# Optimization experiments

Hardware: AMD Instinct MI355X
Metric: run time of the kernel (lower is better)

## Reference

```python
import jax, jax.numpy as jnp
import numpy as np

EPS = 1e-4


def _linear_scan(a, b):
    # y_t = a_t * y_{t-1} + b_t ; a: [L], b: [L, d]
    def combine(c1, c2):
        a1, b1 = c1
        a2, b2 = c2
        return a1 * a2, a2[..., None] * b1 + b2
    _, y = jax.lax.associative_scan(combine, (a, b))
    return y


def setup_inputs() -> dict:
    key = jax.random.key(0)
    k1, k2, k3 = jax.random.split(key, 3)
    L_inner, d, n_seqs = 131072, 512, 8
    h_flat = jax.random.normal(k1, (L_inner, d), dtype=jnp.float32)
    p_selected_flat = jax.random.uniform(k2, (L_inner,), dtype=jnp.float32)
    # outer stream: alternating boundary mask -> cumsum-1 indexes stay in [0, L_inner-1]
    b_flat = jnp.tile(jnp.array([1, 0], dtype=jnp.int32), L_inner)  # [2*L_inner]
    h_seq_idx = jnp.sort(jax.random.randint(k3, (1, L_inner), 0, n_seqs)).astype(jnp.int32)
    return {"h_flat": h_flat, "b_flat": b_flat,
            "p_selected_flat": p_selected_flat, "h_seq_idx": h_seq_idx}


def reference(h_flat, b_flat, p_selected_flat, h_seq_idx):
    # dt derivation: p clamped, dt = -log(1-p); x = h / dt (cast round-trip as in torch)
    p = jnp.clip(p_selected_flat.astype(jnp.float32), EPS, 1.0 - EPS)
    dt = -jnp.log1p(-p)                                   # [L]
    x = (h_flat.astype(jnp.float32) / dt[:, None]).astype(h_flat.dtype).astype(jnp.float32)
    # mamba_chunk_scan_combined with A=-1, B=p, C=1, dstate=1 reduces to:
    #   state_t = exp(-dt_t) * state_{t-1} + dt_t * p_t * x_t ; y_t = state_t
    # with state reset at seq_idx segment boundaries.
    seq = h_seq_idx[0]
    start = jnp.concatenate([jnp.array([True]), seq[1:] != seq[:-1]])
    a = jnp.where(start, 0.0, jnp.exp(-dt))               # decay (== 1-p), reset at starts
    b = (dt * p)[:, None] * x                             # [L, d] input term (== p*h)
    z_bar = _linear_scan(a, b).astype(h_flat.dtype)       # [L_inner, d]
    # dechunk expand: each outer token reads the state of its latest chunk
    idx = jnp.cumsum(b_flat) - 1                          # [L_outer]
    return z_bar[idx]
```

## Files before the change

kernel.cpp:

```cpp
#include <hip/hip_runtime.h>
#include <math.h>

#define EPSV 1e-4f
#define SCHUNK 64

__device__ __forceinline__ float agent_load_f(const float* p) {
    return __hip_atomic_load(p, __ATOMIC_RELAXED, __HIP_MEMORY_SCOPE_AGENT);
}
__device__ __forceinline__ void agent_store_f(float* p, float v) {
    __hip_atomic_store(p, v, __ATOMIC_RELAXED, __HIP_MEMORY_SCOPE_AGENT);
}
__device__ __forceinline__ int agent_load_i(const int* p) {
    return __hip_atomic_load(p, __ATOMIC_RELAXED, __HIP_MEMORY_SCOPE_AGENT);
}
__device__ __forceinline__ void agent_store_i(int* p, int v) {
    __hip_atomic_store(p, v, __ATOMIC_RELAXED, __HIP_MEMORY_SCOPE_AGENT);
}

__global__ void clear_kernel(int* __restrict__ flags, int n) {
    int i = blockIdx.x * blockDim.x + threadIdx.x;
    if (i < n) flags[i] = 0;
}

__global__ void scan_sum_kernel(const int* __restrict__ b, int n,
                                int* __restrict__ bsum) {
    __shared__ int red[256];
    int tid = threadIdx.x;
    int base = blockIdx.x * 1024 + tid * 4;
    int s = 0;
#pragma unroll
    for (int k = 0; k < 4; ++k) {
        int j = base + k;
        if (j < n) s += b[j];
    }
    red[tid] = s;
    __syncthreads();
    for (int off = 128; off > 0; off >>= 1) {
        if (tid < off) red[tid] += red[tid + off];
        __syncthreads();
    }
    if (tid == 0) bsum[blockIdx.x] = red[0];
}

__global__ void scan_offsets_kernel(const int* __restrict__ bsum,
                                    int* __restrict__ boff, int nb) {
    __shared__ int sh[1024];
    int i = threadIdx.x;
    int v = (i < nb) ? bsum[i] : 0;
    sh[i] = v;
    __syncthreads();
    for (int off = 1; off < 1024; off <<= 1) {
        int t = sh[i];
        if (i >= off) t += sh[i - off];
        __syncthreads();
        sh[i] = t;
        __syncthreads();
    }
    if (i < nb) boff[i] = sh[i] - v;
}

__global__ void scan_emit_kernel(const int* __restrict__ b, int n,
                                 const int* __restrict__ boff,
                                 int* __restrict__ sidx, int L, int Louter) {
    __shared__ int red[256];
    int tid = threadIdx.x;
    int base = blockIdx.x * 1024 + tid * 4;
    int v[4];
    int s = 0;
#pragma unroll
    for (int k = 0; k < 4; ++k) {
        int j = base + k;
        v[k] = (j < n) ? b[j] : 0;
        s += v[k];
    }
    red[tid] = s;
    __syncthreads();
    for (int off = 1; off < 256; off <<= 1) {
        int t = red[tid];
        if (tid >= off) t += red[tid - off];
        __syncthreads();
        red[tid] = t;
        __syncthreads();
    }
    int cum = red[tid] - s + boff[blockIdx.x];
#pragma unroll
    for (int k = 0; k < 4; ++k) {
        int j = base + k;
        if (j < n) {
            cum += v[k];
            if (v[k] > 0) {
                int t = cum - 1;
                if (t >= 0 && t < L) sidx[t] = j;
            }
        }
    }
    if (base == 0 && blockIdx.x == 0) sidx[L] = Louter;
}

__global__ __launch_bounds__(512, 4) void scan_lookback_kernel(
        const float* __restrict__ h,
        const float* __restrict__ psel,
        const int* __restrict__ seq,
        const int* __restrict__ sidx,
        float* __restrict__ out,
        float* __restrict__ aggE,
        float* __restrict__ aggP,
        int* __restrict__ flags,
        int L, int d, int Louter, int NC) {
    __shared__ float sh_a[SCHUNK];
    __shared__ float sh_p[SCHUNK];
    __shared__ float sh_A[SCHUNK];
    __shared__ int   sh_j[SCHUNK + 1];
    __shared__ int   sh_g;
    __shared__ float sh_Pbr;

    const int tid = threadIdx.x;
    if (tid == 0) sh_g = atomicAdd(&flags[NC], 1);
    __syncthreads();
    const int g  = sh_g;
    const int t0 = g * SCHUNK;
    const int nt = min(SCHUNK, L - t0);

    if (tid < nt) {
        int t = t0 + tid;
        float p = psel[t];
        p = fminf(fmaxf(p, EPSV), 1.0f - EPSV);
        bool start = (t == 0) || (seq[t] != seq[t - 1]);
        sh_a[tid] = start ? 0.0f : (1.0f - p);
        sh_p[tid] = p;
    }
    if (tid <= nt) sh_j[tid] = sidx[t0 + tid];
    __syncthreads();

    if (tid < 64) {
        float v = (tid < nt) ? sh_a[tid] : 1.0f;
#pragma unroll
        for (int off = 1; off < 64; off <<= 1) {
            float w = __shfl_up(v, off);
            if (tid >= off) v *= w;
        }
        sh_A[tid] = v;
    }
    __syncthreads();

    const int c = tid;
    const float* __restrict__ hp = h + (size_t)t0 * d + c;
    const bool full = (nt == SCHUNK);

    float z[SCHUNK];
    float st = 0.0f;
    if (full) {
#pragma unroll
        for (int grp = 0; grp < SCHUNK / 8; ++grp) {
            float hb[8];
#pragma unroll
            for (int k = 0; k < 8; ++k)
                hb[k] = __builtin_nontemporal_load(hp + (size_t)(grp * 8 + k) * d);
#pragma unroll
            for (int k = 0; k < 8; ++k) {
                int t = grp * 8 + k;
                st = fmaf(sh_a[t], st, sh_p[t] * hb[k]);
                z[t] = st;
            }
        }
    } else {
        for (int t = 0; t < nt; ++t)
            st = fmaf(sh_a[t], st, sh_p[t] * hp[(size_t)t * d]);
    }

    agent_store_f(&aggE[(size_t)g * d + c], st);
    __syncthreads();
    if (tid == 0) {
        agent_store_f(&aggP[g], sh_A[nt - 1]);
        asm volatile("s_waitcnt vmcnt(0)" ::: "memory");
        agent_store_i(&flags[g], 1);
    }

    float carry = 0.0f;
    float prodAcc = 1.0f;
    for (int i = g - 1; i >= 0; --i) {
        if (tid == 0) {
            while (agent_load_i(&flags[i]) == 0) __builtin_amdgcn_s_sleep(1);
            sh_Pbr = agent_load_f(&aggP[i]);
        }
        __syncthreads();
        float Pi = sh_Pbr;
        carry = fmaf(prodAcc, agent_load_f(&aggE[(size_t)i * d + c]), carry);
        prodAcc *= Pi;
        __syncthreads();
        if (prodAcc == 0.0f) break;
    }

    if (full) {
#pragma unroll
        for (int t = 0; t < SCHUNK; ++t) {
            float y = fmaf(sh_A[t], carry, z[t]);
            int j0 = max(sh_j[t], 0);
            int j1 = min(sh_j[t + 1], Louter);
            for (int j = j0; j < j1; ++j)
                __builtin_nontemporal_store(y, out + (size_t)j * d + c);
        }
    } else {
        float s2 = carry;
        for (int t = 0; t < nt; ++t) {
            s2 = fmaf(sh_a[t], s2, sh_p[t] * hp[(size_t)t * d]);
            int j0 = max(sh_j[t], 0);
            int j1 = min(sh_j[t + 1], Louter);
            for (int j = j0; j < j1; ++j)
                out[(size_t)j * d + c] = s2;
        }
    }
}

extern "C" void kernel_launch(void* const* d_in, const int* in_sizes, int n_in,
                              void* d_out, int out_size, void* d_ws, size_t ws_size,
                              hipStream_t stream) {
    const float* h     = (const float*)d_in[0];
    const int*   bflat = (const int*)d_in[1];
    const float* psel  = (const float*)d_in[2];
    const int*   seq   = (const int*)d_in[3];
    float* out = (float*)d_out;

    const int L      = in_sizes[2];
    const int Louter = in_sizes[1];
    const int d      = in_sizes[0] / L;

    const int NC = (L + SCHUNK - 1) / SCHUNK;
    const int nb = (Louter + 1023) / 1024;

    char* ws = (char*)d_ws;
    size_t off = 0;
    auto alloc = [&](size_t bytes) -> void* {
        void* p = ws + off;
        off = (off + bytes + 255) & ~(size_t)255;
        return p;
    };
    float* aggE  = (float*)alloc((size_t)NC * d * 4);
    float* aggP  = (float*)alloc((size_t)NC * 4);
    int*   flags = (int*)alloc((size_t)(NC + 1) * 4);
    int*   bsum  = (int*)alloc((size_t)nb * 4);
    int*   boff  = (int*)alloc((size_t)nb * 4);
    int*   sidx  = (int*)alloc((size_t)(L + 1) * 4);
    (void)ws_size;

    clear_kernel<<<(NC + 1 + 255) / 256, 256, 0, stream>>>(flags, NC + 1);

    scan_sum_kernel<<<nb, 256, 0, stream>>>(bflat, Louter, bsum);
    scan_offsets_kernel<<<1, 1024, 0, stream>>>(bsum, boff, nb);
    scan_emit_kernel<<<nb, 256, 0, stream>>>(bflat, Louter, boff, sidx, L, Louter);

    scan_lookback_kernel<<<NC, d, 0, stream>>>(h, psel, seq, sidx, out,
                                               aggE, aggP, flags,
                                               L, d, Louter, NC);
}
```

Before: 181.2 us.

## Fuse boundary-index scan into the lookback scan kernel

Removes the three separate prefix-sum kernels that build the outer-to-inner index map and folds that work into the main scan kernel. The first blocks by ticket each scan a 1024-element slice of the boundary mask, publish partial sums with flags, and write sidx. All blocks wait on a done counter before reading sidx for their output expansion. This saves kernel launches and lets the index scan overlap with the state scan. In exchange it adds spin-waits, a larger shared-memory footprint, and a grid-wide dependency whose safety relies on ticket ordering.

Result: no change. 182.5 us (+0.7%).

```diff
diff --git a/kernel.cpp b/kernel.cpp
--- a/kernel.cpp
+++ b/kernel.cpp
@@ -22,104 +22,82 @@
     if (i < n) flags[i] = 0;
 }
 
-__global__ void scan_sum_kernel(const int* __restrict__ b, int n,
-                                int* __restrict__ bsum) {
-    __shared__ int red[256];
-    int tid = threadIdx.x;
-    int base = blockIdx.x * 1024 + tid * 4;
-    int s = 0;
-#pragma unroll
-    for (int k = 0; k < 4; ++k) {
-        int j = base + k;
-        if (j < n) s += b[j];
-    }
-    red[tid] = s;
-    __syncthreads();
-    for (int off = 128; off > 0; off >>= 1) {
-        if (tid < off) red[tid] += red[tid + off];
-        __syncthreads();
-    }
-    if (tid == 0) bsum[blockIdx.x] = red[0];
-}
-
-__global__ void scan_offsets_kernel(const int* __restrict__ bsum,
-                                    int* __restrict__ boff, int nb) {
-    __shared__ int sh[1024];
-    int i = threadIdx.x;
-    int v = (i < nb) ? bsum[i] : 0;
-    sh[i] = v;
-    __syncthreads();
-    for (int off = 1; off < 1024; off <<= 1) {
-        int t = sh[i];
-        if (i >= off) t += sh[i - off];
-        __syncthreads();
-        sh[i] = t;
-        __syncthreads();
-    }
-    if (i < nb) boff[i] = sh[i] - v;
-}
-
-__global__ void scan_emit_kernel(const int* __restrict__ b, int n,
-                                 const int* __restrict__ boff,
-                                 int* __restrict__ sidx, int L, int Louter) {
-    __shared__ int red[256];
-    int tid = threadIdx.x;
-    int base = blockIdx.x * 1024 + tid * 4;
-    int v[4];
-    int s = 0;
-#pragma unroll
-    for (int k = 0; k < 4; ++k) {
-        int j = base + k;
-        v[k] = (j < n) ? b[j] : 0;
-        s += v[k];
-    }
-    red[tid] = s;
-    __syncthreads();
-    for (int off = 1; off < 256; off <<= 1) {
-        int t = red[tid];
-        if (tid >= off) t += red[tid - off];
-        __syncthreads();
-        red[tid] = t;
-        __syncthreads();
-    }
-    int cum = red[tid] - s + boff[blockIdx.x];
-#pragma unroll
-    for (int k = 0; k < 4; ++k) {
-        int j = base + k;
-        if (j < n) {
-            cum += v[k];
-            if (v[k] > 0) {
-                int t = cum - 1;
-                if (t >= 0 && t < L) sidx[t] = j;
-            }
-        }
-    }
-    if (base == 0 && blockIdx.x == 0) sidx[L] = Louter;
-}
-
-__global__ __launch_bounds__(512, 4) void scan_lookback_kernel(
+__global__ __launch_bounds__(512, 4) void fused_scan_kernel(
         const float* __restrict__ h,
+        const int*   __restrict__ bflat,
         const float* __restrict__ psel,
-        const int* __restrict__ seq,
-        const int* __restrict__ sidx,
+        const int*   __restrict__ seq,
         float* __restrict__ out,
         float* __restrict__ aggE,
         float* __restrict__ aggP,
-        int* __restrict__ flags,
-        int L, int d, int Louter, int NC) {
+        int*   __restrict__ flags,
+        int*   __restrict__ bsum,
+        int*   __restrict__ sidx,
+        int L, int d, int Louter, int NC, int nsb) {
     __shared__ float sh_a[SCHUNK];
     __shared__ float sh_p[SCHUNK];
     __shared__ float sh_A[SCHUNK];
     __shared__ int   sh_j[SCHUNK + 1];
     __shared__ int   sh_g;
     __shared__ float sh_Pbr;
+    __shared__ int   red[512];
+    __shared__ int   red2[512];
+
+    int* ticket = flags + NC;
+    int* done   = flags + NC + 1;
+    int* bflags = flags + NC + 2;
 
     const int tid = threadIdx.x;
-    if (tid == 0) sh_g = atomicAdd(&flags[NC], 1);
+    if (tid == 0) sh_g = atomicAdd(ticket, 1);
     __syncthreads();
     const int g  = sh_g;
     const int t0 = g * SCHUNK;
     const int nt = min(SCHUNK, L - t0);
+
+    for (int s = g; s < nsb; s += NC) {
+        int base = s * 1024 + tid * 2;
+        int v0 = (base     < Louter) ? bflat[base]     : 0;
+        int v1 = (base + 1 < Louter) ? bflat[base + 1] : 0;
+        int ssum = v0 + v1;
+        red[tid] = ssum;
+        __syncthreads();
+        for (int off = 1; off < 512; off <<= 1) {
+            int tv = red[tid];
+            if (tid >= off) tv += red[tid - off];
+            __syncthreads();
+            red[tid] = tv;
+            __syncthreads();
+        }
+        if (tid == 511) {
+            agent_store_i(&bsum[s], red[511]);
+            asm volatile("s_waitcnt vmcnt(0)" ::: "memory");
+            agent_store_i(&bflags[s], 1);
+        }
+        int pre = 0;
+        if (tid < s) {
+            while (agent_load_i(&bflags[tid]) == 0) __builtin_amdgcn_s_sleep(1);
+            pre = agent_load_i(&bsum[tid]);
+        }
+        red2[tid] = pre;
+        __syncthreads();
+        for (int off = 256; off > 0; off >>= 1) {
+            if (tid < off) red2[tid] += red2[tid + off];
+            __syncthreads();
+        }
+        int cum = red[tid] - ssum + red2[0];
+        cum += v0;
+        if (v0 > 0 && cum - 1 >= 0 && cum - 1 < L)
+            agent_store_i(&sidx[cum - 1], base);
+        cum += v1;
+        if (v1 > 0 && cum - 1 >= 0 && cum - 1 < L)
+            agent_store_i(&sidx[cum - 1], base + 1);
+        if (s == 0 && tid == 0)
+            agent_store_i(&sidx[L], Louter);
+    }
+    if (g < nsb) {
+        __syncthreads();
+        if (tid == 0) atomicAdd(done, 1);
+    }
 
     if (tid < nt) {
         int t = t0 + tid;
@@ -129,7 +107,6 @@
         sh_a[tid] = start ? 0.0f : (1.0f - p);
         sh_p[tid] = p;
     }
-    if (tid <= nt) sh_j[tid] = sidx[t0 + tid];
     __syncthreads();
 
     if (tid < 64) {
@@ -190,6 +167,13 @@
         __syncthreads();
         if (prodAcc == 0.0f) break;
     }
+
+    if (tid == 0) {
+        while (agent_load_i(done) < nsb) __builtin_amdgcn_s_sleep(8);
+    }
+    __syncthreads();
+    if (tid <= nt) sh_j[tid] = agent_load_i(&sidx[t0 + tid]);
+    __syncthreads();
 
     if (full) {
 #pragma unroll
@@ -225,8 +209,8 @@
     const int Louter = in_sizes[1];
     const int d      = in_sizes[0] / L;
 
-    const int NC = (L + SCHUNK - 1) / SCHUNK;
-    const int nb = (Louter + 1023) / 1024;
+    const int NC  = (L + SCHUNK - 1) / SCHUNK;
+    const int nsb = (Louter + 1023) / 1024;
 
     char* ws = (char*)d_ws;
     size_t off = 0;
@@ -237,19 +221,15 @@
     };
     float* aggE  = (float*)alloc((size_t)NC * d * 4);
     float* aggP  = (float*)alloc((size_t)NC * 4);
-    int*   flags = (int*)alloc((size_t)(NC + 1) * 4);
-    int*   bsum  = (int*)alloc((size_t)nb * 4);
-    int*   boff  = (int*)alloc((size_t)nb * 4);
+    int*   flags = (int*)alloc((size_t)(NC + 2 + nsb) * 4);
+    int*   bsum  = (int*)alloc((size_t)nsb * 4);
     int*   sidx  = (int*)alloc((size_t)(L + 1) * 4);
     (void)ws_size;
 
-    clear_kernel<<<(NC + 1 + 255) / 256, 256, 0, stream>>>(flags, NC + 1);
-
-    scan_sum_kernel<<<nb, 256, 0, stream>>>(bflat, Louter, bsum);
-    scan_offsets_kernel<<<1, 1024, 0, stream>>>(bsum, boff, nb);
-    scan_emit_kernel<<<nb, 256, 0, stream>>>(bflat, Louter, boff, sidx, L, Louter);
-
-    scan_lookback_kernel<<<NC, d, 0, stream>>>(h, psel, seq, sidx, out,
-                                               aggE, aggP, flags,
-                                               L, d, Louter, NC);
-}
+    const int nclr = NC + 2 + nsb;
+    clear_kernel<<<(nclr + 255) / 256, 256, 0, stream>>>(flags, nclr);
+
+    fused_scan_kernel<<<NC, d, 0, stream>>>(h, bflat, psel, seq, out,
+                                            aggE, aggP, flags, bsum, sidx,
+                                            L, d, Louter, NC, nsb);
+}
```
